# Optimization experiments

Hardware: AMD Instinct MI355X
Metric: run time of the kernel (lower is better)

## Reference

```python
import jax, jax.numpy as jnp
import numpy as np
import math

EPS = 1e-6
TEMPERATURE = 1.0
NEG = -100.0


def setup_inputs() -> dict:
    key = jax.random.key(0)
    k1, k2, k3 = jax.random.split(key, 3)
    B, N, C = 16, 2048, 64
    x = jax.random.normal(k1, (B, N, C), dtype=jnp.float32)
    y = jax.random.normal(k2, (B, N, C), dtype=jnp.float32)
    # complementary keep / pruned gates, as produced by the TPS token scorer
    keep = jax.random.bernoulli(k3, 0.5, (B, N, 1)).astype(jnp.float32)
    pruned = 1.0 - keep
    return {
        "x": x,
        "y": y,
        "current_keep_decision": keep,
        "current_pruned_decision": pruned,
    }


def reference(x, y, current_keep_decision, current_pruned_decision):
    # Training branch of TPSModule.forward (module defaults to training mode).
    B, N, C = x.shape
    # --- get_sim(x, None, mask_eye=-100, l2_norm=True) ---
    xn = x / (jnp.linalg.norm(x, axis=-1, keepdims=True) + EPS)
    sim = jnp.einsum("bnc,bmc->bnm", xn, xn)  # [B, N, N]
    eye = jnp.eye(N, dtype=bool)
    sim = jnp.where(eye[None, :, :], NEG, sim)
    sim = sim / TEMPERATURE
    # mask out columns of non-kept tokens
    keep_b = current_keep_decision.reshape(B, 1, N).astype(bool)
    sim = jnp.where(keep_b, sim, NEG)
    # hard top-1 (with ties) per row, gated by pruned flag of the source row
    sim_th = jnp.max(sim, axis=2, keepdims=True)  # [B, N, 1]
    mask = (sim == sim_th).astype(x.dtype) * current_pruned_decision  # [B, N, N]
    cos = mask * sim
    # transpose: now rows index destination (kept) tokens
    mask_t = mask.transpose(0, 2, 1)
    cos_t = cos.transpose(0, 2, 1)
    numerator = jnp.exp(cos_t) * mask_t  # [B, N, N]
    denominator = math.e + jnp.sum(numerator, axis=-1, keepdims=True)  # [B, N, 1]
    out = x * (math.e / denominator) + jnp.einsum(
        "bnm,bmc->bnc", numerator / denominator, x
    )
    return out
```

## Files before the change

### kernel.cpp

```cpp
#include <hip/hip_runtime.h>
#include <math.h>

#define BB 16
#define NN 2048
#define CC 64
#define TPB 256
#define MAXT 72
#define IVN (MAXT * 16)
#define E_CONST 2.71828182845904523536f

typedef __attribute__((ext_vector_type(8))) short bf16x8;
typedef __attribute__((ext_vector_type(4))) float f32x4;
#define MFMA(A_, B_, C_) __builtin_amdgcn_mfma_f32_16x16x32_bf16(A_, B_, C_, 0, 0, 0)

__device__ __forceinline__ unsigned short rnbf16(float v) {
    unsigned u = __float_as_uint(v);
    return (unsigned short)((u + 0x7FFFu + ((u >> 16) & 1u)) >> 16);
}
__device__ __forceinline__ float bf2f(unsigned short h) {
    return __uint_as_float((unsigned)h << 16);
}

__global__ __launch_bounds__(TPB) void k_pre(const float* __restrict__ keep,
                                             float* __restrict__ outz,
                                             float* __restrict__ S,
                                             int* __restrict__ cntP,
                                             int* __restrict__ cntK,
                                             int* __restrict__ listP,
                                             int* __restrict__ listK) {
    const int tid = threadIdx.x, lane = tid & 63;

    float4* o4 = (float4*)outz + (size_t)blockIdx.x * 1024;
    float4 z = {0.0f, 0.0f, 0.0f, 0.0f};
#pragma unroll
    for (int i = 0; i < 4; ++i) o4[i * TPB + tid] = z;

    const int b = blockIdx.x;
    if (b >= BB) return;

    __shared__ int cP, cK;
    if (tid == 0) { cP = 0; cK = 0; }
    __syncthreads();
    for (int i = tid; i < NN; i += TPB) S[b * NN + i] = 0.0f;
    const unsigned long long lt = (lane == 63) ? 0x7fffffffffffffffull
                                               : ((1ull << lane) - 1ull);
#pragma unroll
    for (int it = 0; it < NN / TPB; ++it) {
        int n = it * TPB + tid;
        bool kp = keep[b * NN + n] != 0.0f;
        unsigned long long mk = __ballot(kp);
        int nk = __popcll(mk);
        int bk = 0, bp = 0;
        if (lane == 0) {
            bk = atomicAdd(&cK, nk);
            bp = atomicAdd(&cP, 64 - nk);
        }
        bk = __shfl(bk, 0); bp = __shfl(bp, 0);
        int pk = __popcll(mk & lt);
        if (kp) listK[b * NN + bk + pk] = n;
        else    listP[b * NN + bp + (lane - pk)] = n;
    }
    __syncthreads();
    if (tid == 0) { cntP[b] = cP; cntK[b] = cK; }
}

__global__ __launch_bounds__(TPB) void k_pack(const float* __restrict__ x,
                                              const int* __restrict__ cntK,
                                              const int* __restrict__ listK,
                                              float4* __restrict__ colA,
                                              const int* __restrict__ cntP,
                                              const int* __restrict__ listP,
                                              float4* __restrict__ rowB,
                                              float* __restrict__ ivrArr) {
    int id = blockIdx.x;
    const bool isA = id < BB * MAXT;
    if (!isA) id -= BB * MAXT;
    const int b = id & 15;
    const int t = id >> 4;
    const int C = isA ? cntK[b] : cntP[b];
    const int* __restrict__ list = isA ? listK : listP;
    float4* __restrict__ outF = isA ? colA : rowB;

    const int lane = threadIdx.x & 63;
    const int wid  = threadIdx.x >> 6;
    __shared__ float4 stage4[384];
    unsigned short* st = (unsigned short*)stage4;
    const float* xb = x + (size_t)b * NN * CC;

    const int g  = (lane >> 3) & 3;
    const int kf = lane >> 5;
    const int e  = lane & 7;
#pragma unroll
    for (int it = 0; it < 4; ++it) {
        int ci = wid * 4 + it;
        int cp = t * 16 + ci;
        float v = 0.0f;
        if (cp < C) {
            int tok = list[b * NN + cp];
            float xv = xb[(size_t)tok * CC + lane];
            float sq = xv * xv;
#pragma unroll
            for (int off = 32; off; off >>= 1) sq += __shfl_xor(sq, off, 64);
            float ivr = 1.0f / (sqrtf(sq) + 1e-6f);
            if (!isA && lane == 0) ivrArr[b * IVN + cp] = ivr;
            v = isA ? xv * ivr : xv;
        }
        unsigned short hb = rnbf16(v);
        float r1 = v - bf2f(hb);
        unsigned short mb = rnbf16(r1);
        float r2 = r1 - bf2f(mb);
        unsigned short lb = rnbf16(r2);
        int lt = ci + g * 16;
        st[((0 + kf) * 64 + lt) * 8 + e] = hb;
        st[((2 + kf) * 64 + lt) * 8 + e] = mb;
        st[((4 + kf) * 64 + lt) * 8 + e] = lb;
    }
    __syncthreads();
    float4* dst = outF + (size_t)(b * MAXT + t) * 384;
    for (int i = threadIdx.x; i < 384; i += TPB) dst[i] = stage4[i];
}

__device__ __forceinline__ void loadA6(const float4* __restrict__ af, int lane,
                                       bf16x8& h0, bf16x8& h1, bf16x8& m0,
                                       bf16x8& m1, bf16x8& l0, bf16x8& l1) {
    h0 = __builtin_bit_cast(bf16x8, af[0 * 64 + lane]);
    h1 = __builtin_bit_cast(bf16x8, af[1 * 64 + lane]);
    m0 = __builtin_bit_cast(bf16x8, af[2 * 64 + lane]);
    m1 = __builtin_bit_cast(bf16x8, af[3 * 64 + lane]);
    l0 = __builtin_bit_cast(bf16x8, af[4 * 64 + lane]);
    l1 = __builtin_bit_cast(bf16x8, af[5 * 64 + lane]);
}

__device__ __forceinline__ void computeTile(
    bf16x8 A0h, bf16x8 A1h, bf16x8 A0m, bf16x8 A1m, bf16x8 A0l, bf16x8 A1l,
    bf16x8 B0h, bf16x8 B1h, bf16x8 B0m, bf16x8 B1m, bf16x8 B0l, bf16x8 B1l,
    int t, int i, int K, int cgrp,
    float& tmax, unsigned long long& mskA, unsigned long long& mskB) {
    f32x4 accS = {0.f, 0.f, 0.f, 0.f}, accH = {0.f, 0.f, 0.f, 0.f};
    accS = MFMA(A0m, B0m, accS); accS = MFMA(A1m, B1m, accS);
    accS = MFMA(A0h, B0l, accS); accS = MFMA(A1h, B1l, accS);
    accS = MFMA(A0l, B0h, accS); accS = MFMA(A1l, B1h, accS);
    accH = MFMA(A0h, B0m, accH); accH = MFMA(A1h, B1m, accH);
    accH = MFMA(A0m, B0h, accH); accH = MFMA(A1m, B1h, accH);
    accH = MFMA(A0h, B0h, accH); accH = MFMA(A1h, B1h, accH);

    const int cb = t * 16 + cgrp;
    const int ib = (i & 15) << 2;
#pragma unroll
    for (int j = 0; j < 4; ++j) {
        float s = accH[j] + accS[j];
        s = (cb + j < K) ? s : -3.0e38f;
        unsigned long long bit = 1ull << (ib | j);
        if (i < 16) {
            if (s > tmax)       { tmax = s; mskA = bit; mskB = 0ull; }
            else if (s == tmax)  mskA |= bit;
        } else {
            if (s > tmax)       { tmax = s; mskB = bit; mskA = 0ull; }
            else if (s == tmax)  mskB |= bit;
        }
    }
}

__global__ __launch_bounds__(TPB) void k_argmax(
    const float* __restrict__ x,
    const float4* __restrict__ colA,
    const float4* __restrict__ rowB,
    const float* __restrict__ ivrArr,
    const int* __restrict__ cntP, const int* __restrict__ cntK,
    const int* __restrict__ listP, const int* __restrict__ listK,
    float* __restrict__ S,
    float* __restrict__ A) {

    const int b  = blockIdx.x & 15;
    const int rt = blockIdx.x >> 4;
    const int P = cntP[b], K = cntK[b];
    const int base = rt * 16;
    if (base >= P) return;

    const int lane = threadIdx.x & 63;
    const int wid  = threadIdx.x >> 6;

    const float4* rb = rowB + (size_t)(b * MAXT + rt) * 384;
    bf16x8 B0h, B1h, B0m, B1m, B0l, B1l;
    loadA6(rb, lane, B0h, B1h, B0m, B1m, B0l, B1l);

    float tmax = -3.0e38f;
    unsigned long long mskA = 0ull, mskB = 0ull;
    const int NT = (K + 15) >> 4;
    const float4* ca = colA + (size_t)b * MAXT * 384;
    const int cgrp = (lane >> 4) << 2;

    const int ntw = (NT - wid + 3) >> 2;
    bf16x8 Aa0h, Aa1h, Aa0m, Aa1m, Aa0l, Aa1l;
    bf16x8 Ab0h, Ab1h, Ab0m, Ab1m, Ab0l, Ab1l;

    if (ntw > 0)
        loadA6(ca + (size_t)wid * 384, lane, Aa0h, Aa1h, Aa0m, Aa1m, Aa0l, Aa1l);
    int k = 0;
    while (k < ntw) {
        if (k + 1 < ntw)
            loadA6(ca + (size_t)(wid + 4 * (k + 1)) * 384, lane,
                   Ab0h, Ab1h, Ab0m, Ab1m, Ab0l, Ab1l);
        computeTile(Aa0h, Aa1h, Aa0m, Aa1m, Aa0l, Aa1l,
                    B0h, B1h, B0m, B1m, B0l, B1l,
                    wid + 4 * k, k, K, cgrp, tmax, mskA, mskB);
        ++k;
        if (k >= ntw) break;
        if (k + 1 < ntw)
            loadA6(ca + (size_t)(wid + 4 * (k + 1)) * 384, lane,
                   Aa0h, Aa1h, Aa0m, Aa1m, Aa0l, Aa1l);
        computeTile(Ab0h, Ab1h, Ab0m, Ab1m, Ab0l, Ab1l,
                    B0h, B1h, B0m, B1m, B0l, B1l,
                    wid + 4 * k, k, K, cgrp, tmax, mskA, mskB);
        ++k;
    }

    float m = tmax;
    m = fmaxf(m, __shfl_xor(m, 16, 64));
    m = fmaxf(m, __shfl_xor(m, 32, 64));
    __shared__ float mW[16][4];
    if (lane < 16) mW[lane][wid] = m;
    __syncthreads();

    const int nvr = min(16, P - base);
    for (int r = 0; r < nvr; ++r) {
        float M = fmaxf(fmaxf(mW[r][0], mW[r][1]), fmaxf(mW[r][2], mW[r][3]));
        unsigned long long bal = __ballot((lane & 15) == r && tmax == M);
        if (bal == 0ull) continue;
        int src = listP[b * NN + base + r];
        float ivr = ivrArr[b * IVN + base + r];
        float wgt = expf(M * ivr);
        float xv = x[((size_t)b * NN + src) * CC + lane];
        while (bal) {
            int sl = __ffsll(bal) - 1;
            bal &= bal - 1;
            unsigned long long mA = __shfl(mskA, sl);
            unsigned long long mB = __shfl(mskB, sl);
            int cg = (sl >> 4) << 2;
            while (mA) {
                int bb = __ffsll(mA) - 1; mA &= mA - 1;
                int colp = (wid + 4 * (bb >> 2)) * 16 + cg + (bb & 3);
                int dst = listK[b * NN + colp];
                atomicAdd(&A[((size_t)b * NN + dst) * CC + lane], wgt * xv);
                if (lane == 0) atomicAdd(&S[b * NN + dst], wgt);
            }
            while (mB) {
                int bb = __ffsll(mB) - 1; mB &= mB - 1;
                int colp = (wid + 4 * (16 + (bb >> 2))) * 16 + cg + (bb & 3);
                int dst = listK[b * NN + colp];
                atomicAdd(&A[((size_t)b * NN + dst) * CC + lane], wgt * xv);
                if (lane == 0) atomicAdd(&S[b * NN + dst], wgt);
            }
        }
    }
}

__global__ __launch_bounds__(TPB) void k_finalize(const float* __restrict__ x,
                                                  const float* __restrict__ S,
                                                  float* __restrict__ out) {
    int i = blockIdx.x * TPB + threadIdx.x;
    int row = i >> 4;
    float inv = 1.0f / (E_CONST + S[row]);
    float4 xv = ((const float4*)x)[i];
    float4 av = ((float4*)out)[i];
    float4 o;
    o.x = (xv.x * E_CONST + av.x) * inv;
    o.y = (xv.y * E_CONST + av.y) * inv;
    o.z = (xv.z * E_CONST + av.z) * inv;
    o.w = (xv.w * E_CONST + av.w) * inv;
    ((float4*)out)[i] = o;
}

extern "C" void kernel_launch(void* const* d_in, const int* in_sizes, int n_in,
                              void* d_out, int out_size, void* d_ws, size_t ws_size,
                              hipStream_t stream) {
    const float* x    = (const float*)d_in[0];
    const float* keep = (const float*)d_in[2];
    float* out = (float*)d_out;

    char* ws = (char*)d_ws;
    float* S     = (float*)(ws + (128 << 10));
    int*   cntP  = (int*)(ws + (256 << 10));
    int*   cntK  = cntP + 16;
    int*   listP = (int*)(ws + (256 << 10) + 128);
    int*   listK = listP + BB * NN;
    float* ivrArr = (float*)(ws + (768 << 10));
    float4* colA = (float4*)(ws + (1 << 20));
    float4* rowB = (float4*)(ws + (8 << 20));

    k_pre<<<512, TPB, 0, stream>>>(keep, out, S, cntP, cntK, listP, listK);

    k_pack<<<2 * BB * MAXT, TPB, 0, stream>>>(x, cntK, listK, colA,
                                              cntP, listP, rowB, ivrArr);

    k_argmax<<<2048, TPB, 0, stream>>>(x, colA, rowB, ivrArr,
                                       cntP, cntK, listP, listK, S, out);

    k_finalize<<<(BB * NN * CC / 4) / TPB, TPB, 0, stream>>>(x, S, out);
}
```

Baseline: 122.8 us.

## Process two row tiles per argmax block with 512 threads, drop manual double-buffering

```diff
diff --git a/kernel.cpp b/kernel.cpp
--- a/kernel.cpp
+++ b/kernel.cpp
@@ -5,6 +5,7 @@
 #define NN 2048
 #define CC 64
 #define TPB 256
+#define TPA 512
 #define MAXT 72
 #define IVN (MAXT * 16)
 #define E_CONST 2.71828182845904523536f
@@ -120,7 +121,7 @@
     for (int i = threadIdx.x; i < 384; i += TPB) dst[i] = stage4[i];
 }
 
-__device__ __forceinline__ void loadA6(const float4* __restrict__ af, int lane,
+__device__ __forceinline__ void loadF6(const float4* __restrict__ af, int lane,
                                        bf16x8& h0, bf16x8& h1, bf16x8& m0,
                                        bf16x8& m1, bf16x8& l0, bf16x8& l1) {
     h0 = __builtin_bit_cast(bf16x8, af[0 * 64 + lane]);
@@ -131,37 +132,7 @@
     l1 = __builtin_bit_cast(bf16x8, af[5 * 64 + lane]);
 }
 
-__device__ __forceinline__ void computeTile(
-    bf16x8 A0h, bf16x8 A1h, bf16x8 A0m, bf16x8 A1m, bf16x8 A0l, bf16x8 A1l,
-    bf16x8 B0h, bf16x8 B1h, bf16x8 B0m, bf16x8 B1m, bf16x8 B0l, bf16x8 B1l,
-    int t, int i, int K, int cgrp,
-    float& tmax, unsigned long long& mskA, unsigned long long& mskB) {
-    f32x4 accS = {0.f, 0.f, 0.f, 0.f}, accH = {0.f, 0.f, 0.f, 0.f};
-    accS = MFMA(A0m, B0m, accS); accS = MFMA(A1m, B1m, accS);
-    accS = MFMA(A0h, B0l, accS); accS = MFMA(A1h, B1l, accS);
-    accS = MFMA(A0l, B0h, accS); accS = MFMA(A1l, B1h, accS);
-    accH = MFMA(A0h, B0m, accH); accH = MFMA(A1h, B1m, accH);
-    accH = MFMA(A0m, B0h, accH); accH = MFMA(A1m, B1h, accH);
-    accH = MFMA(A0h, B0h, accH); accH = MFMA(A1h, B1h, accH);
-
-    const int cb = t * 16 + cgrp;
-    const int ib = (i & 15) << 2;
-#pragma unroll
-    for (int j = 0; j < 4; ++j) {
-        float s = accH[j] + accS[j];
-        s = (cb + j < K) ? s : -3.0e38f;
-        unsigned long long bit = 1ull << (ib | j);
-        if (i < 16) {
-            if (s > tmax)       { tmax = s; mskA = bit; mskB = 0ull; }
-            else if (s == tmax)  mskA |= bit;
-        } else {
-            if (s > tmax)       { tmax = s; mskB = bit; mskA = 0ull; }
-            else if (s == tmax)  mskB |= bit;
-        }
-    }
-}
-
-__global__ __launch_bounds__(TPB) void k_argmax(
+__global__ __launch_bounds__(TPA) void k_argmax(
     const float* __restrict__ x,
     const float4* __restrict__ colA,
     const float4* __restrict__ rowB,
@@ -174,15 +145,18 @@
     const int b  = blockIdx.x & 15;
     const int rt = blockIdx.x >> 4;
     const int P = cntP[b], K = cntK[b];
-    const int base = rt * 16;
+    const int base = rt * 32;
     if (base >= P) return;
 
-    const int lane = threadIdx.x & 63;
-    const int wid  = threadIdx.x >> 6;
-
-    const float4* rb = rowB + (size_t)(b * MAXT + rt) * 384;
+    const int tid  = threadIdx.x;
+    const int lane = tid & 63;
+    const int wid  = tid >> 6;
+    const int cs   = wid >> 1;
+    const int h    = wid & 1;
+
+    const float4* rb = rowB + (size_t)(b * MAXT + 2 * rt + h) * 384;
     bf16x8 B0h, B1h, B0m, B1m, B0l, B1l;
-    loadA6(rb, lane, B0h, B1h, B0m, B1m, B0l, B1l);
+    loadF6(rb, lane, B0h, B1h, B0m, B1m, B0l, B1l);
 
     float tmax = -3.0e38f;
     unsigned long long mskA = 0ull, mskB = 0ull;
@@ -190,42 +164,49 @@
     const float4* ca = colA + (size_t)b * MAXT * 384;
     const int cgrp = (lane >> 4) << 2;
 
-    const int ntw = (NT - wid + 3) >> 2;
-    bf16x8 Aa0h, Aa1h, Aa0m, Aa1m, Aa0l, Aa1l;
-    bf16x8 Ab0h, Ab1h, Ab0m, Ab1m, Ab0l, Ab1l;
-
-    if (ntw > 0)
-        loadA6(ca + (size_t)wid * 384, lane, Aa0h, Aa1h, Aa0m, Aa1m, Aa0l, Aa1l);
-    int k = 0;
-    while (k < ntw) {
-        if (k + 1 < ntw)
-            loadA6(ca + (size_t)(wid + 4 * (k + 1)) * 384, lane,
-                   Ab0h, Ab1h, Ab0m, Ab1m, Ab0l, Ab1l);
-        computeTile(Aa0h, Aa1h, Aa0m, Aa1m, Aa0l, Aa1l,
-                    B0h, B1h, B0m, B1m, B0l, B1l,
-                    wid + 4 * k, k, K, cgrp, tmax, mskA, mskB);
-        ++k;
-        if (k >= ntw) break;
-        if (k + 1 < ntw)
-            loadA6(ca + (size_t)(wid + 4 * (k + 1)) * 384, lane,
-                   Aa0h, Aa1h, Aa0m, Aa1m, Aa0l, Aa1l);
-        computeTile(Ab0h, Ab1h, Ab0m, Ab1m, Ab0l, Ab1l,
-                    B0h, B1h, B0m, B1m, B0l, B1l,
-                    wid + 4 * k, k, K, cgrp, tmax, mskA, mskB);
-        ++k;
+    int i = 0;
+    for (int t = cs; t < NT; t += 4, ++i) {
+        const float4* af = ca + (size_t)t * 384;
+        bf16x8 A0h, A1h, A0m, A1m, A0l, A1l;
+        loadF6(af, lane, A0h, A1h, A0m, A1m, A0l, A1l);
+
+        f32x4 accS = {0.f, 0.f, 0.f, 0.f}, accH = {0.f, 0.f, 0.f, 0.f};
+        accS = MFMA(A0m, B0m, accS); accS = MFMA(A1m, B1m, accS);
+        accS = MFMA(A0h, B0l, accS); accS = MFMA(A1h, B1l, accS);
+        accS = MFMA(A0l, B0h, accS); accS = MFMA(A1l, B1h, accS);
+        accH = MFMA(A0h, B0m, accH); accH = MFMA(A1h, B1m, accH);
+        accH = MFMA(A0m, B0h, accH); accH = MFMA(A1m, B1h, accH);
+        accH = MFMA(A0h, B0h, accH); accH = MFMA(A1h, B1h, accH);
+
+        const int cb = t * 16 + cgrp;
+        const int ib = (i & 15) << 2;
+#pragma unroll
+        for (int j = 0; j < 4; ++j) {
+            float s = accH[j] + accS[j];
+            s = (cb + j < K) ? s : -3.0e38f;
+            unsigned long long bit = 1ull << (ib | j);
+            if (i < 16) {
+                if (s > tmax)       { tmax = s; mskA = bit; mskB = 0ull; }
+                else if (s == tmax)  mskA |= bit;
+            } else {
+                if (s > tmax)       { tmax = s; mskB = bit; mskA = 0ull; }
+                else if (s == tmax)  mskB |= bit;
+            }
+        }
     }
 
     float m = tmax;
     m = fmaxf(m, __shfl_xor(m, 16, 64));
     m = fmaxf(m, __shfl_xor(m, 32, 64));
-    __shared__ float mW[16][4];
-    if (lane < 16) mW[lane][wid] = m;
-    __syncthreads();
-
-    const int nvr = min(16, P - base);
+    __shared__ float mW[32][4];
+    if (lane < 16) mW[h * 16 + lane][cs] = m;
+    __syncthreads();
+
+    const int nvr = min(32, P - base);
     for (int r = 0; r < nvr; ++r) {
+        if ((r >> 4) != h) continue;
         float M = fmaxf(fmaxf(mW[r][0], mW[r][1]), fmaxf(mW[r][2], mW[r][3]));
-        unsigned long long bal = __ballot((lane & 15) == r && tmax == M);
+        unsigned long long bal = __ballot((lane & 15) == (r & 15) && tmax == M);
         if (bal == 0ull) continue;
         int src = listP[b * NN + base + r];
         float ivr = ivrArr[b * IVN + base + r];
@@ -239,14 +220,14 @@
             int cg = (sl >> 4) << 2;
             while (mA) {
                 int bb = __ffsll(mA) - 1; mA &= mA - 1;
-                int colp = (wid + 4 * (bb >> 2)) * 16 + cg + (bb & 3);
+                int colp = (cs + 4 * (bb >> 2)) * 16 + cg + (bb & 3);
                 int dst = listK[b * NN + colp];
                 atomicAdd(&A[((size_t)b * NN + dst) * CC + lane], wgt * xv);
                 if (lane == 0) atomicAdd(&S[b * NN + dst], wgt);
             }
             while (mB) {
                 int bb = __ffsll(mB) - 1; mB &= mB - 1;
-                int colp = (wid + 4 * (16 + (bb >> 2))) * 16 + cg + (bb & 3);
+                int colp = (cs + 4 * (16 + (bb >> 2))) * 16 + cg + (bb & 3);
                 int dst = listK[b * NN + colp];
                 atomicAdd(&A[((size_t)b * NN + dst) * CC + lane], wgt * xv);
                 if (lane == 0) atomicAdd(&S[b * NN + dst], wgt);
@@ -293,7 +274,7 @@
     k_pack<<<2 * BB * MAXT, TPB, 0, stream>>>(x, cntK, listK, colA,
                                               cntP, listP, rowB, ivrArr);
 
-    k_argmax<<<2048, TPB, 0, stream>>>(x, colA, rowB, ivrArr,
+    k_argmax<<<1024, TPA, 0, stream>>>(x, colA, rowB, ivrArr,
                                        cntP, cntK, listP, listK, S, out);
 
     k_finalize<<<(BB * NN * CC / 4) / TPB, TPB, 0, stream>>>(x, S, out);
```

Measured after the change: 120.7 us. Within noise of the previous version (-1.7%).
